# Kernel tuning notes

Hardware: AMD Instinct MI355X
Metric: run time of the kernel (lower is better)

## Reference

```python
import jax, jax.numpy as jnp
import numpy as np

ALPHA = 0.2  # LeakyReLU negative slope (init arg alpha)


def setup_inputs() -> dict:
    key = jax.random.key(0)
    k1, k2, k3 = jax.random.split(key, 3)
    B, N, F_in, F_out = 8, 2048, 256, 256
    inp = jax.random.normal(k1, (B, N, F_in), dtype=jnp.float32)
    adj = jnp.ones((B, N, N), dtype=jnp.float32)  # unused by the module's forward
    # xavier_uniform with gain=1.414
    gain = 1.414
    bW = gain * np.sqrt(6.0 / (F_in + F_out))
    W = jax.random.uniform(k2, (F_in, F_out), minval=-bW, maxval=bW, dtype=jnp.float32)
    ba = gain * np.sqrt(6.0 / (2 * F_out + 1))
    a = jax.random.uniform(k3, (2 * F_out, 1), minval=-ba, maxval=ba, dtype=jnp.float32)
    return {"inp": inp, "adj": adj, "W": W, "a": a}


def reference(inp, adj, W, a):
    # inp: [B, N, F_in]; W: [F_in, F_out]; a: [2*F_out, 1]. adj is unused (as in source).
    F_out = W.shape[1]
    h = jnp.matmul(inp, W)  # [B, N, F_out]
    # e[b,i,j] = leakyrelu(a1 . h_i + a2 . h_j)  (equivalent to the repeat+cat+matmul)
    a1 = a[:F_out, 0]
    a2 = a[F_out:, 0]
    s1 = jnp.einsum('bnf,f->bn', h, a1)  # [B, N]
    s2 = jnp.einsum('bnf,f->bn', h, a2)  # [B, N]
    e = jax.nn.leaky_relu(s1[:, :, None] + s2[:, None, :], negative_slope=ALPHA)  # [B, N, N]
    # global per-batch min-max normalization, then affine *30 - 20
    mn = jnp.min(e, axis=(1, 2), keepdims=True)
    mx = jnp.max(e, axis=(1, 2), keepdims=True)
    e = (e - mn) / (mx - mn) * 30.0 - 20.0
    attention = jax.nn.sigmoid(e)  # dropout p=0 / eval: identity
    h_prime = jnp.matmul(attention, h)  # [B, N, F_out]
    h_prime = jax.nn.elu(h_prime)  # concat=True branch
    return h_prime, attention
```

## Files before the change

### kernel.cpp

```cpp
#include <hip/hip_runtime.h>
#include <stdint.h>

#define B_   8
#define N_   2048
#define F_   256
#define BN_  (B_ * N_)
#define ALPHA_ 0.2f

typedef __attribute__((ext_vector_type(8))) short  short8;
typedef __attribute__((ext_vector_type(4))) float  f32x4;

__device__ __forceinline__ unsigned short f2bf(float x) {
  uint32_t u = __float_as_uint(x);
  uint32_t r = (u + 0x7fffu + ((u >> 16) & 1u)) >> 16;
  return (unsigned short)r;
}

__device__ __forceinline__ uint32_t fkey(float f) {
  uint32_t b = __float_as_uint(f);
  return b ^ (uint32_t)(((int32_t)b >> 31) | (int32_t)0x80000000);
}
__device__ __forceinline__ float ikey(uint32_t k) {
  uint32_t b = (k & 0x80000000u) ? (k ^ 0x80000000u) : ~k;
  return __uint_as_float(b);
}

__device__ __forceinline__ void nt_store4(float* p, f32x4 v) {
  __builtin_nontemporal_store(v, (f32x4*)p);
}

__device__ __forceinline__ short8 pack8(float4 a, float4 b) {
  short8 s;
  s[0] = (short)f2bf(a.x); s[1] = (short)f2bf(a.y);
  s[2] = (short)f2bf(a.z); s[3] = (short)f2bf(a.w);
  s[4] = (short)f2bf(b.x); s[5] = (short)f2bf(b.y);
  s[6] = (short)f2bf(b.z); s[7] = (short)f2bf(b.w);
  return s;
}

__global__ void k_cvt_w(const float* __restrict__ W, unsigned short* __restrict__ WT) {
  int k = blockIdx.x, n = threadIdx.x;
  WT[n * F_ + k] = f2bf(W[k * F_ + n]);
}

__launch_bounds__(256, 2)
__global__ void k_gemm1(const float* __restrict__ inp,
                        const unsigned short* __restrict__ WT,
                        const float* __restrict__ avec,
                        unsigned short* __restrict__ hT,
                        float* __restrict__ s1g, float* __restrict__ s2g,
                        uint32_t* __restrict__ maxk, uint32_t* __restrict__ mink) {
  __shared__ __align__(16) unsigned short Trans[256 * 48];
  __shared__ float s1_lds[32], s2_lds[32];

  const int tid  = threadIdx.x;
  const int wave = tid >> 6, lane = tid & 63;
  const int n16  = lane & 15, quad = lane >> 4;
  const int i0   = blockIdx.x * 32;
  const int b    = i0 >> 11;

  if (tid < 32) { s1_lds[tid] = 0.0f; s2_lds[tid] = 0.0f; }
  __syncthreads();

  f32x4 acc[2][4];
  #pragma unroll
  for (int mt = 0; mt < 2; ++mt)
    #pragma unroll
    for (int nt = 0; nt < 4; ++nt) acc[mt][nt] = (f32x4){0.f, 0.f, 0.f, 0.f};

  const float* ap0 = inp + (size_t)(i0 + n16) * F_ + quad * 8;
  const float* ap1 = ap0 + (size_t)16 * F_;
  const unsigned short* bp = WT + (size_t)(wave * 64 + n16) * F_ + quad * 8;

  #pragma unroll 2
  for (int k0 = 0; k0 < F_; k0 += 32) {
    float4 a00 = *(const float4*)(ap0 + k0);
    float4 a01 = *(const float4*)(ap0 + k0 + 4);
    float4 a10 = *(const float4*)(ap1 + k0);
    float4 a11 = *(const float4*)(ap1 + k0 + 4);
    short8 bf_[4];
    #pragma unroll
    for (int nt = 0; nt < 4; ++nt)
      bf_[nt] = *(const short8*)(bp + (size_t)nt * 16 * F_ + k0);
    short8 af0 = pack8(a00, a01);
    short8 af1 = pack8(a10, a11);
    #pragma unroll
    for (int nt = 0; nt < 4; ++nt) {
      acc[0][nt] = __builtin_amdgcn_mfma_f32_16x16x32_bf16(af0, bf_[nt], acc[0][nt], 0, 0, 0);
      acc[1][nt] = __builtin_amdgcn_mfma_f32_16x16x32_bf16(af1, bf_[nt], acc[1][nt], 0, 0, 0);
    }
  }

  #pragma unroll
  for (int mt = 0; mt < 2; ++mt)
    #pragma unroll
    for (int nt = 0; nt < 4; ++nt) {
      int f = (wave << 6) + (nt << 4) + n16;
      int i = (mt << 4) + (quad << 2);
      ushort4 pk;
      pk.x = f2bf(acc[mt][nt][0]); pk.y = f2bf(acc[mt][nt][1]);
      pk.z = f2bf(acc[mt][nt][2]); pk.w = f2bf(acc[mt][nt][3]);
      *(ushort4*)(Trans + f * 48 + i) = pk;
    }

  float a1v[4], a2v[4];
  #pragma unroll
  for (int nt = 0; nt < 4; ++nt) {
    int f = (wave << 6) + (nt << 4) + n16;
    a1v[nt] = avec[f];
    a2v[nt] = avec[F_ + f];
  }
  #pragma unroll
  for (int mt = 0; mt < 2; ++mt) {
    float s1p[4] = {0, 0, 0, 0}, s2p[4] = {0, 0, 0, 0};
    #pragma unroll
    for (int nt = 0; nt < 4; ++nt)
      #pragma unroll
      for (int rg = 0; rg < 4; ++rg) {
        s1p[rg] = fmaf(acc[mt][nt][rg], a1v[nt], s1p[rg]);
        s2p[rg] = fmaf(acc[mt][nt][rg], a2v[nt], s2p[rg]);
      }
    #pragma unroll
    for (int rg = 0; rg < 4; ++rg) {
      float v1 = s1p[rg], v2 = s2p[rg];
      #pragma unroll
      for (int off = 1; off < 16; off <<= 1) {
        v1 += __shfl_xor(v1, off);
        v2 += __shfl_xor(v2, off);
      }
      if (n16 == 0) {
        atomicAdd(&s1_lds[(mt << 4) + (quad << 2) + rg], v1);
        atomicAdd(&s2_lds[(mt << 4) + (quad << 2) + rg], v2);
      }
    }
  }
  __syncthreads();

  #pragma unroll
  for (int pass = 0; pass < 4; ++pass) {
    int f = pass * 64 + wave * 16 + (lane >> 2);
    int i = (lane & 3) * 8;
    short8 v = *(const short8*)(Trans + f * 48 + i);
    *(short8*)(hT + (size_t)f * BN_ + i0 + i) = v;
  }

  if (tid < 32) {
    float v1 = s1_lds[tid], v2 = s2_lds[tid];
    s1g[i0 + tid] = v1;
    s2g[i0 + tid] = v2;
    float mn1 = v1, mx1 = v1, mn2 = v2, mx2 = v2;
    #pragma unroll
    for (int off = 1; off < 32; off <<= 1) {
      mn1 = fminf(mn1, __shfl_xor(mn1, off));
      mx1 = fmaxf(mx1, __shfl_xor(mx1, off));
      mn2 = fminf(mn2, __shfl_xor(mn2, off));
      mx2 = fmaxf(mx2, __shfl_xor(mx2, off));
    }
    if (tid == 0) {
      atomicMax(&maxk[b * 2 + 0], fkey(mx1));
      atomicMax(&maxk[b * 2 + 1], fkey(mx2));
      atomicMin(&mink[b * 2 + 0], fkey(mn1));
      atomicMin(&mink[b * 2 + 1], fkey(mn2));
    }
  }
}

__launch_bounds__(256, 2)
__global__ void k_gemm2(const unsigned short* __restrict__ hT,
                        const float* __restrict__ s1, const float* __restrict__ s2,
                        const uint32_t* __restrict__ maxk, const uint32_t* __restrict__ mink,
                        float* __restrict__ hprime,
                        float* __restrict__ att) {
  __shared__ __align__(16) unsigned short Atile[2][1024];

  const int tid  = threadIdx.x;
  const int wave = tid >> 6, lane = tid & 63;
  const int n16  = lane & 15, quad = lane >> 4;
  const int blk  = blockIdx.x;
  const int b    = blk & 7;
  const int i0   = (blk >> 3) * 32;

  float mx1 = ikey(maxk[b * 2 + 0]), mx2 = ikey(maxk[b * 2 + 1]);
  float mn1 = ikey(mink[b * 2 + 0]), mn2 = ikey(mink[b * 2 + 1]);
  float smn = mn1 + mn2, smx = mx1 + mx2;
  float emn = fmaxf(smn, ALPHA_ * smn);
  float emx = fmaxf(smx, ALPHA_ * smx);
  float scale  = 30.0f / (emx - emn);
  const float uscale = -scale;
  const float ubias  = emn * scale + 20.0f;

  const int r_att = tid >> 3;
  const int c_att = tid & 7;
  const float s1v = s1[b * N_ + i0 + r_att];
  const float* s2b = s2 + b * N_;
  float* attrow = att + ((size_t)(b * N_ + i0 + r_att)) * N_;

  const int wbyte  = r_att * 64 + ((c_att * 8) ^ ((r_att & 3) << 4));
  const int rbyte0 = n16 * 64 + ((quad * 16) ^ ((n16 & 3) << 4));
  const int rbyte1 = rbyte0 + 16 * 64;

  const unsigned short* bp = hT + (size_t)(wave * 64 + n16) * BN_ + (size_t)b * N_ + quad * 8;

  f32x4 acc[2][4];
  #pragma unroll
  for (int mt = 0; mt < 2; ++mt)
    #pragma unroll
    for (int nt = 0; nt < 4; ++nt) acc[mt][nt] = (f32x4){0.f, 0.f, 0.f, 0.f};

  int buf = 0;
  for (int k0 = 0; k0 < N_; k0 += 32, buf ^= 1) {
    short8 bf_[4];
    bf_[0] = *(const short8*)(bp + k0);
    bf_[1] = *(const short8*)(bp + (size_t)16 * BN_ + k0);
    bf_[2] = *(const short8*)(bp + (size_t)32 * BN_ + k0);
    bf_[3] = *(const short8*)(bp + (size_t)48 * BN_ + k0);

    float4 va = *(const float4*)(s2b + k0 + c_att * 4);
    float v[4] = {va.x, va.y, va.z, va.w};
    #pragma unroll
    for (int jj = 0; jj < 4; ++jj) {
      float s = s1v + v[jj];
      float l = fmaxf(s, ALPHA_ * s);
      float u = fmaf(l, uscale, ubias);
      float p_ = __builtin_amdgcn_rcpf(1.0f + __expf(u));
      v[jj] = p_;
    }
    nt_store4(attrow + k0 + c_att * 4, (f32x4){v[0], v[1], v[2], v[3]});
    ushort4 spk;
    spk.x = f2bf(v[0]); spk.y = f2bf(v[1]); spk.z = f2bf(v[2]); spk.w = f2bf(v[3]);
    *(ushort4*)((char*)Atile + buf * 2048 + wbyte) = spk;

    asm volatile("s_waitcnt lgkmcnt(0)" ::: "memory");
    __builtin_amdgcn_s_barrier();
    asm volatile("" ::: "memory");

    short8 af0 = *(const short8*)((const char*)Atile + buf * 2048 + rbyte0);
    short8 af1 = *(const short8*)((const char*)Atile + buf * 2048 + rbyte1);

    #pragma unroll
    for (int nt = 0; nt < 4; ++nt) {
      acc[0][nt] = __builtin_amdgcn_mfma_f32_16x16x32_bf16(af0, bf_[nt], acc[0][nt], 0, 0, 0);
      acc[1][nt] = __builtin_amdgcn_mfma_f32_16x16x32_bf16(af1, bf_[nt], acc[1][nt], 0, 0, 0);
    }
  }

  float* hp = hprime + ((size_t)(b * N_ + i0)) * F_;
  #pragma unroll
  for (int mt = 0; mt < 2; ++mt)
    #pragma unroll
    for (int nt = 0; nt < 4; ++nt) {
      int fcol = (wave << 6) + (nt << 4) + n16;
      int irow = (mt << 4) + (quad << 2);
      #pragma unroll
      for (int rg = 0; rg < 4; ++rg) {
        float x = acc[mt][nt][rg];
        float y = x > 0.0f ? x : (__expf(x) - 1.0f);
        __builtin_nontemporal_store(y, hp + (size_t)(irow + rg) * F_ + fcol);
      }
    }
}

extern "C" void kernel_launch(void* const* d_in, const int* in_sizes, int n_in,
                              void* d_out, int out_size, void* d_ws, size_t ws_size,
                              hipStream_t stream) {
  const float* inp  = (const float*)d_in[0];
  const float* W    = (const float*)d_in[2];
  const float* avec = (const float*)d_in[3];

  float* hprime = (float*)d_out;
  float* att    = (float*)d_out + (size_t)B_ * N_ * F_;

  char* ws = (char*)d_ws;
  unsigned short* WT = (unsigned short*)ws;
  unsigned short* hT = (unsigned short*)(ws + 131072);
  float* s1          = (float*)(ws + 131072 + 8388608);
  float* s2          = s1 + BN_;
  uint32_t* maxk     = (uint32_t*)(s2 + BN_);
  uint32_t* mink     = maxk + 16;

  (void)hipMemsetAsync(maxk, 0x00, 64, stream);
  (void)hipMemsetAsync(mink, 0xFF, 64, stream);

  k_cvt_w<<<F_, F_, 0, stream>>>(W, WT);
  k_gemm1<<<BN_ / 32, 256, 0, stream>>>(inp, WT, avec, hT, s1, s2, maxk, mink);
  k_gemm2<<<512, 256, 0, stream>>>(hT, s1, s2, maxk, mink, hprime, att);
}
```

Baseline: 311.3 us.

## Stage GEMM operands through LDS with async global-to-LDS loads and multi-buffering

Both GEMM kernels now stage the B operand (WT or hT) into LDS using global_load_lds async copies. gemm1 is double-buffered and gemm2 triple-buffered, with vmcnt-based waits so the next tiles load while the current MFMAs run. gemm2 also preloads the whole s2 row into LDS, and gemm1 converts its A operand to bf16 in LDS. The two memsets are folded into the weight-conversion kernel. In exchange, gemm2 uses far more LDS, which may lower occupancy, and the A-tile XOR swizzle was dropped, which may bring back bank conflicts.

After: 276.9 us. -11.0%, faster.

```diff
diff --git a/kernel.cpp b/kernel.cpp
--- a/kernel.cpp
+++ b/kernel.cpp
@@ -25,21 +25,20 @@
   return __uint_as_float(b);
 }
 
+__device__ __forceinline__ void async_load16(const void* g, void* l) {
+  __builtin_amdgcn_global_load_lds(
+      (const __attribute__((address_space(1))) uint32_t*)g,
+      (__attribute__((address_space(3))) uint32_t*)l, 16, 0, 0);
+}
+
 __device__ __forceinline__ void nt_store4(float* p, f32x4 v) {
   __builtin_nontemporal_store(v, (f32x4*)p);
 }
 
-__device__ __forceinline__ short8 pack8(float4 a, float4 b) {
-  short8 s;
-  s[0] = (short)f2bf(a.x); s[1] = (short)f2bf(a.y);
-  s[2] = (short)f2bf(a.z); s[3] = (short)f2bf(a.w);
-  s[4] = (short)f2bf(b.x); s[5] = (short)f2bf(b.y);
-  s[6] = (short)f2bf(b.z); s[7] = (short)f2bf(b.w);
-  return s;
-}
-
-__global__ void k_cvt_w(const float* __restrict__ W, unsigned short* __restrict__ WT) {
+__global__ void k_cvt_w(const float* __restrict__ W, unsigned short* __restrict__ WT,
+                        uint32_t* __restrict__ maxk, uint32_t* __restrict__ mink) {
   int k = blockIdx.x, n = threadIdx.x;
+  if (k == 0 && n < 16) { maxk[n] = 0u; mink[n] = 0xFFFFFFFFu; }
   WT[n * F_ + k] = f2bf(W[k * F_ + n]);
 }
 
@@ -50,7 +49,7 @@
                         unsigned short* __restrict__ hT,
                         float* __restrict__ s1g, float* __restrict__ s2g,
                         uint32_t* __restrict__ maxk, uint32_t* __restrict__ mink) {
-  __shared__ __align__(16) unsigned short Trans[256 * 48];
+  __shared__ __align__(16) char smem[4096 + 32768];
   __shared__ float s1_lds[32], s2_lds[32];
 
   const int tid  = threadIdx.x;
@@ -60,7 +59,29 @@
   const int b    = i0 >> 11;
 
   if (tid < 32) { s1_lds[tid] = 0.0f; s2_lds[tid] = 0.0f; }
-  __syncthreads();
+
+  const int ar = tid >> 3, ac = tid & 7;
+
+  auto stage_b = [&](int buf_, int k0_) {
+    #pragma unroll
+    for (int g4 = 0; g4 < 4; ++g4) {
+      int f = (wave << 6) + (g4 << 4) + (lane >> 2);
+      int p = lane & 3;
+      async_load16(WT + (size_t)f * F_ + k0_ + p * 8,
+                   smem + 4096 + buf_ * 16384 + wave * 4096 + g4 * 1024);
+    }
+  };
+
+  {
+    float4 va = *(const float4*)(inp + (size_t)(i0 + ar) * F_ + ac * 4);
+    stage_b(0, 0);
+    ushort4 pk;
+    pk.x = f2bf(va.x); pk.y = f2bf(va.y); pk.z = f2bf(va.z); pk.w = f2bf(va.w);
+    *(ushort4*)(smem + ar * 64 + ac * 8) = pk;
+  }
+  asm volatile("s_waitcnt vmcnt(0) lgkmcnt(0)" ::: "memory");
+  __builtin_amdgcn_s_barrier();
+  asm volatile("" ::: "memory");
 
   f32x4 acc[2][4];
   #pragma unroll
@@ -68,28 +89,43 @@
     #pragma unroll
     for (int nt = 0; nt < 4; ++nt) acc[mt][nt] = (f32x4){0.f, 0.f, 0.f, 0.f};
 
-  const float* ap0 = inp + (size_t)(i0 + n16) * F_ + quad * 8;
-  const float* ap1 = ap0 + (size_t)16 * F_;
-  const unsigned short* bp = WT + (size_t)(wave * 64 + n16) * F_ + quad * 8;
-
   #pragma unroll 2
-  for (int k0 = 0; k0 < F_; k0 += 32) {
-    float4 a00 = *(const float4*)(ap0 + k0);
-    float4 a01 = *(const float4*)(ap0 + k0 + 4);
-    float4 a10 = *(const float4*)(ap1 + k0);
-    float4 a11 = *(const float4*)(ap1 + k0 + 4);
+  for (int t = 0; t < 8; ++t) {
+    const int cur = t & 1;
+    const int k0n = (t + 1) << 5;
+
+    float4 va;
+    if (t < 7) {
+      va = *(const float4*)(inp + (size_t)(i0 + ar) * F_ + k0n + ac * 4);
+      stage_b(cur ^ 1, k0n);
+    }
+
+    short8 af0 = *(const short8*)(smem + cur * 2048 + n16 * 64 + quad * 16);
+    short8 af1 = *(const short8*)(smem + cur * 2048 + (16 + n16) * 64 + quad * 16);
     short8 bf_[4];
     #pragma unroll
     for (int nt = 0; nt < 4; ++nt)
-      bf_[nt] = *(const short8*)(bp + (size_t)nt * 16 * F_ + k0);
-    short8 af0 = pack8(a00, a01);
-    short8 af1 = pack8(a10, a11);
+      bf_[nt] = *(const short8*)(smem + 4096 + cur * 16384 +
+                                 (wave * 64 + nt * 16 + n16) * 64 + quad * 16);
+
+    if (t < 7) {
+      ushort4 pk;
+      pk.x = f2bf(va.x); pk.y = f2bf(va.y); pk.z = f2bf(va.z); pk.w = f2bf(va.w);
+      *(ushort4*)(smem + (cur ^ 1) * 2048 + ar * 64 + ac * 8) = pk;
+    }
+
     #pragma unroll
     for (int nt = 0; nt < 4; ++nt) {
       acc[0][nt] = __builtin_amdgcn_mfma_f32_16x16x32_bf16(af0, bf_[nt], acc[0][nt], 0, 0, 0);
       acc[1][nt] = __builtin_amdgcn_mfma_f32_16x16x32_bf16(af1, bf_[nt], acc[1][nt], 0, 0, 0);
     }
-  }
+
+    asm volatile("s_waitcnt vmcnt(0) lgkmcnt(0)" ::: "memory");
+    __builtin_amdgcn_s_barrier();
+    asm volatile("" ::: "memory");
+  }
+
+  unsigned short* Trans = (unsigned short*)smem;
 
   #pragma unroll
   for (int mt = 0; mt < 2; ++mt)
@@ -171,7 +207,9 @@
                         const uint32_t* __restrict__ maxk, const uint32_t* __restrict__ mink,
                         float* __restrict__ hprime,
                         float* __restrict__ att) {
+  __shared__ __align__(16) unsigned short Btile[3][256 * 32];
   __shared__ __align__(16) unsigned short Atile[2][1024];
+  __shared__ __align__(16) float s2_lds[N_];
 
   const int tid  = threadIdx.x;
   const int wave = tid >> 6, lane = tid & 63;
@@ -195,11 +233,25 @@
   const float* s2b = s2 + b * N_;
   float* attrow = att + ((size_t)(b * N_ + i0 + r_att)) * N_;
 
-  const int wbyte  = r_att * 64 + ((c_att * 8) ^ ((r_att & 3) << 4));
-  const int rbyte0 = n16 * 64 + ((quad * 16) ^ ((n16 & 3) << 4));
-  const int rbyte1 = rbyte0 + 16 * 64;
-
-  const unsigned short* bp = hT + (size_t)(wave * 64 + n16) * BN_ + (size_t)b * N_ + quad * 8;
+  auto stage_b = [&](int slot, int k0_) {
+    #pragma unroll
+    for (int g4 = 0; g4 < 4; ++g4) {
+      int f = (wave << 6) + (g4 << 4) + (lane >> 2);
+      int p = lane & 3;
+      async_load16(hT + (size_t)f * BN_ + b * N_ + k0_ + p * 8,
+                   (char*)Btile + slot * 16384 + wave * 4096 + g4 * 1024);
+    }
+  };
+
+  #pragma unroll
+  for (int it = 0; it < 2; ++it)
+    async_load16(s2b + wave * 512 + it * 256 + lane * 4,
+                 (char*)s2_lds + wave * 2048 + it * 1024);
+  stage_b(0, 0);
+  stage_b(1, 32);
+  asm volatile("s_waitcnt vmcnt(8)" ::: "memory");
+  __builtin_amdgcn_s_barrier();
+  asm volatile("" ::: "memory");
 
   f32x4 acc[2][4];
   #pragma unroll
@@ -207,15 +259,12 @@
     #pragma unroll
     for (int nt = 0; nt < 4; ++nt) acc[mt][nt] = (f32x4){0.f, 0.f, 0.f, 0.f};
 
-  int buf = 0;
-  for (int k0 = 0; k0 < N_; k0 += 32, buf ^= 1) {
-    short8 bf_[4];
-    bf_[0] = *(const short8*)(bp + k0);
-    bf_[1] = *(const short8*)(bp + (size_t)16 * BN_ + k0);
-    bf_[2] = *(const short8*)(bp + (size_t)32 * BN_ + k0);
-    bf_[3] = *(const short8*)(bp + (size_t)48 * BN_ + k0);
-
-    float4 va = *(const float4*)(s2b + k0 + c_att * 4);
+  int sl_r = 0, sl_n = 2;
+  for (int t = 0; t < 64; ++t) {
+    const int abuf = (t & 1) * 2048;
+    const int k0   = t << 5;
+
+    float4 va = *(const float4*)((const char*)s2_lds + k0 * 4 + c_att * 16);
     float v[4] = {va.x, va.y, va.z, va.w};
     #pragma unroll
     for (int jj = 0; jj < 4; ++jj) {
@@ -228,21 +277,33 @@
     nt_store4(attrow + k0 + c_att * 4, (f32x4){v[0], v[1], v[2], v[3]});
     ushort4 spk;
     spk.x = f2bf(v[0]); spk.y = f2bf(v[1]); spk.z = f2bf(v[2]); spk.w = f2bf(v[3]);
-    *(ushort4*)((char*)Atile + buf * 2048 + wbyte) = spk;
-
-    asm volatile("s_waitcnt lgkmcnt(0)" ::: "memory");
+    *(ushort4*)((char*)Atile + abuf + tid * 8) = spk;
+
+    asm volatile("s_waitcnt vmcnt(5) lgkmcnt(0)" ::: "memory");
     __builtin_amdgcn_s_barrier();
     asm volatile("" ::: "memory");
 
-    short8 af0 = *(const short8*)((const char*)Atile + buf * 2048 + rbyte0);
-    short8 af1 = *(const short8*)((const char*)Atile + buf * 2048 + rbyte1);
+    stage_b(sl_n, k0 + 64);
+
+    short8 af0 = *(const short8*)((const char*)Atile + abuf + n16 * 64 + quad * 16);
+    short8 af1 = *(const short8*)((const char*)Atile + abuf + (16 + n16) * 64 + quad * 16);
+    short8 bf_[4];
+    #pragma unroll
+    for (int nt = 0; nt < 4; ++nt)
+      bf_[nt] = *(const short8*)((const char*)Btile + sl_r * 16384 +
+                                 (wave * 64 + nt * 16 + n16) * 64 + quad * 16);
 
     #pragma unroll
     for (int nt = 0; nt < 4; ++nt) {
       acc[0][nt] = __builtin_amdgcn_mfma_f32_16x16x32_bf16(af0, bf_[nt], acc[0][nt], 0, 0, 0);
       acc[1][nt] = __builtin_amdgcn_mfma_f32_16x16x32_bf16(af1, bf_[nt], acc[1][nt], 0, 0, 0);
     }
-  }
+
+    sl_r = (sl_r == 2) ? 0 : sl_r + 1;
+    sl_n = (sl_n == 2) ? 0 : sl_n + 1;
+  }
+
+  asm volatile("s_waitcnt vmcnt(0)" ::: "memory");
 
   float* hp = hprime + ((size_t)(b * N_ + i0)) * F_;
   #pragma unroll
@@ -278,10 +339,7 @@
   uint32_t* maxk     = (uint32_t*)(s2 + BN_);
   uint32_t* mink     = maxk + 16;
 
-  (void)hipMemsetAsync(maxk, 0x00, 64, stream);
-  (void)hipMemsetAsync(mink, 0xFF, 64, stream);
-
-  k_cvt_w<<<F_, F_, 0, stream>>>(W, WT);
+  k_cvt_w<<<F_, F_, 0, stream>>>(W, WT, maxk, mink);
   k_gemm1<<<BN_ / 32, 256, 0, stream>>>(inp, WT, avec, hT, s1, s2, maxk, mink);
   k_gemm2<<<512, 256, 0, stream>>>(hT, s1, s2, maxk, mink, hprime, att);
 }
```
